# Optimization experiments

Hardware: AMD Instinct MI355X
Metric: run time of the kernel (lower is better)

## Reference

```python
import jax, jax.numpy as jnp
import numpy as np

B, C, H, W = 16, 192, 48, 48
EPS = 1e-5  # torch LayerNorm default


def setup_inputs() -> dict:
    key = jax.random.key(0)
    ks = jax.random.split(key, 5)
    dim = C
    x = jax.random.normal(ks[0], (B, C, H, W), dtype=jnp.float32)
    ln_w = jnp.ones((dim,), dtype=jnp.float32)
    ln_b = jnp.zeros((dim,), dtype=jnp.float32)
    s = 1.0 / np.sqrt(dim)
    Wq = jax.random.uniform(ks[1], (dim, dim), jnp.float32, -s, s)
    Wk = jax.random.uniform(ks[2], (dim, dim), jnp.float32, -s, s)
    Wv = jax.random.uniform(ks[3], (dim, dim), jnp.float32, -s, s)
    w1 = jnp.ones((1,), dtype=jnp.float32)
    w2 = jnp.ones((1,), dtype=jnp.float32)
    return {"x": x, "ln_w": ln_w, "ln_b": ln_b, "Wq": Wq, "Wk": Wk, "Wv": Wv, "w1": w1, "w2": w2}


def reference(x, ln_w, ln_b, Wq, Wk, Wv, w1, w2):
    b, c, h, w = x.shape
    # [B, C, H, W] -> [B, N, C]
    xf = x.reshape(b, c, h * w).transpose(0, 2, 1)
    # LayerNorm over channel dim
    mu = jnp.mean(xf, axis=-1, keepdims=True)
    var = jnp.mean(jnp.square(xf - mu), axis=-1, keepdims=True)
    xn = (xf - mu) * jax.lax.rsqrt(var + EPS) * ln_w + ln_b
    # torch Linear: y = x @ W^T
    Q = jnp.einsum('bnc,dc->bnd', xn, Wq)
    K = jnp.einsum('bnc,dc->bnd', xn, Wk)
    V = jnp.einsum('bnc,dc->bnd', xn, Wv)
    S = jnp.einsum('bnd,bmd->bnm', Q, K)  # [B, N, N]
    attn1 = jax.nn.softmax(S, axis=-1)
    attn2 = jnp.square(jax.nn.relu(S))
    # learned blend weights (softmax over two scalars)
    e1, e2 = jnp.exp(w1), jnp.exp(w2)
    denom = e1 + e2
    attn = (e1 / denom) * attn1 + (e2 / denom) * attn2
    out = jnp.einsum('bnm,bmd->bnd', attn, V)  # [B, N, C]
    out = out.transpose(0, 2, 1).reshape(b, c, h, w)
    return out + x
```

## Files before the change

### kernel.cpp

```cpp
#include <hip/hip_runtime.h>

#define NN 2304
#define CC 192
#define NBATCH 16

typedef unsigned short u16;
typedef __bf16 bf16x8 __attribute__((ext_vector_type(8)));
typedef float f32x4 __attribute__((ext_vector_type(4)));
typedef float f32x16 __attribute__((ext_vector_type(16)));

__device__ __forceinline__ u16 bf16bits(float f) {
  union { float f; unsigned u; } v;
  v.f = f;
  unsigned r = v.u + 0x7FFFu + ((v.u >> 16) & 1u);
  return (u16)(r >> 16);
}

__device__ __forceinline__ uint32_t cvtpk(float lo, float hi) {
  uint32_t d;
  asm("v_cvt_pk_bf16_f32 %0, %1, %2" : "=v"(d) : "v"(lo), "v"(hi));
  return d;
}

__device__ __forceinline__ int swzK(int row, int col) {
  int ch = col >> 3;
  int phys = (ch & ~7) | ((ch ^ row) & 7);
  return row * 192 + (phys << 3) + (col & 7);
}
__device__ __forceinline__ int swz64(int row, int col) {
  int ch = (col >> 3) ^ row;
  return (row << 6) | ((ch & 7) << 3) | (col & 7);
}

__device__ __forceinline__ void gll16(const u16* g, u16* l) {
  __builtin_amdgcn_global_load_lds(
      (const __attribute__((address_space(1))) u16*)g,
      (__attribute__((address_space(3))) u16*)l, 16, 0, 0);
}

__global__ __launch_bounds__(256) void ln_kernel(
    const float* __restrict__ x, const float* __restrict__ lnw,
    const float* __restrict__ lnb, u16* __restrict__ xn) {
  __shared__ float xt[192 * 65];
  __shared__ float psum[4][64], psq[4][64];
  __shared__ float mu_s[64], rs_s[64];
  __shared__ float lw_s[192], lb_s[192];
  int t = threadIdx.x;
  int b = blockIdx.y, n0 = blockIdx.x * 64;
  const float* xb = x + (size_t)b * CC * NN;
  if (t < 192) { lw_s[t] = lnw[t]; lb_s[t] = lnb[t]; }
#pragma unroll
  for (int i = 0; i < 48; ++i) {
    int idx = i * 256 + t;
    int c = idx >> 6, n = idx & 63;
    xt[c * 65 + n] = xb[(size_t)c * NN + n0 + n];
  }
  __syncthreads();
  {
    int n = t & 63, part = t >> 6;
    float s = 0.f, s2 = 0.f;
#pragma unroll
    for (int c = part * 48; c < part * 48 + 48; ++c) {
      float v = xt[c * 65 + n];
      s += v; s2 += v * v;
    }
    psum[part][n] = s; psq[part][n] = s2;
  }
  __syncthreads();
  if (t < 64) {
    float s = psum[0][t] + psum[1][t] + psum[2][t] + psum[3][t];
    float s2 = psq[0][t] + psq[1][t] + psq[2][t] + psq[3][t];
    float mu = s * (1.0f / 192.0f);
    float var = s2 * (1.0f / 192.0f) - mu * mu;
    mu_s[t] = mu;
    rs_s[t] = rsqrtf(var + 1e-5f);
  }
  __syncthreads();
#pragma unroll
  for (int i = 0; i < 12; ++i) {
    int u = i * 256 + t;
    int n = u / 48, cq = (u % 48) * 4;
    float mu = mu_s[n], rs = rs_s[n];
    float v0 = (xt[(cq + 0) * 65 + n] - mu) * rs * lw_s[cq + 0] + lb_s[cq + 0];
    float v1 = (xt[(cq + 1) * 65 + n] - mu) * rs * lw_s[cq + 1] + lb_s[cq + 1];
    float v2 = (xt[(cq + 2) * 65 + n] - mu) * rs * lw_s[cq + 2] + lb_s[cq + 2];
    float v3 = (xt[(cq + 3) * 65 + n] - mu) * rs * lw_s[cq + 3] + lb_s[cq + 3];
    uint2 o;
    o.x = cvtpk(v0, v1);
    o.y = cvtpk(v2, v3);
    *(uint2*)&xn[((size_t)(b * NN + n0 + n)) * CC + cq] = o;
  }
}

__global__ __launch_bounds__(256) void wconv_kernel(
    const float* __restrict__ Wq, const float* __restrict__ Wk,
    const float* __restrict__ Wv, u16* __restrict__ wbf) {
  int z = blockIdx.y;
  const float* W = (z == 0) ? Wq : (z == 1 ? Wk : Wv);
  u16* o = wbf + (size_t)z * 36864;
  int idx = (blockIdx.x * 256 + (int)threadIdx.x) * 8;
  float4 f0 = *(const float4*)&W[idx];
  float4 f1 = *(const float4*)&W[idx + 4];
  uint4 v;
  v.x = cvtpk(f0.x, f0.y);
  v.y = cvtpk(f0.z, f0.w);
  v.z = cvtpk(f1.x, f1.y);
  v.w = cvtpk(f1.z, f1.w);
  *(uint4*)&o[idx] = v;
}

__global__ __launch_bounds__(256, 3) void qkv_gemm(
    const u16* __restrict__ xn, const u16* __restrict__ wbf,
    u16* __restrict__ qb, u16* __restrict__ kb, u16* __restrict__ vtb) {
  __shared__ u16 xs[12288];
  __shared__ u16 wsm[12288];
  int t = threadIdx.x, w = t >> 6, lane = t & 63, l15 = lane & 15, qd = lane >> 4;
  int m0 = blockIdx.x * 64, n0 = blockIdx.y * 64;

#pragma unroll
  for (int i = 0; i < 6; ++i) {
    int cid = i * 4 + w, sc = cid * 64 + lane;
    int row = sc / 24, pc = sc % 24;
    int gc = (pc & ~7) | ((pc ^ row) & 7);
    gll16(xn + (size_t)(m0 + row) * 192 + gc * 8, xs + cid * 512);
  }
#pragma unroll
  for (int i = 0; i < 6; ++i) {
    int cid = i * 4 + w, sc = cid * 64 + lane;
    int row = sc / 24, pc = sc % 24;
    int gc = (pc & ~7) | ((pc ^ row) & 7);
    gll16(wbf + (size_t)(n0 + row) * 192 + gc * 8, wsm + cid * 512);
  }

  bf16x8 a[6];
  const f32x4 fz = {0.f, 0.f, 0.f, 0.f};
  for (int z = 0; z < 3; ++z) {
    asm volatile("s_waitcnt vmcnt(0) lgkmcnt(0)\ns_barrier" ::: "memory");
    if (z == 0) {
#pragma unroll
      for (int kk = 0; kk < 6; ++kk)
        a[kk] = *(const bf16x8*)&xs[swzK(w * 16 + l15, kk * 32 + qd * 8)];
    }
    f32x4 acc[4];
#pragma unroll
    for (int ct = 0; ct < 4; ++ct) {
      acc[ct] = fz;
#pragma unroll
      for (int kk = 0; kk < 6; ++kk) {
        bf16x8 bfr = *(const bf16x8*)&wsm[swzK(ct * 16 + l15, kk * 32 + qd * 8)];
        acc[ct] = __builtin_amdgcn_mfma_f32_16x16x32_bf16(a[kk], bfr, acc[ct], 0, 0, 0);
      }
    }
    asm volatile("s_waitcnt lgkmcnt(0)\ns_barrier" ::: "memory");
    if (z < 2) {
#pragma unroll
      for (int i = 0; i < 6; ++i) {
        int cid = i * 4 + w, sc = cid * 64 + lane;
        int row = sc / 24, pc = sc % 24;
        int gc = (pc & ~7) | ((pc ^ row) & 7);
        gll16(wbf + (size_t)(z + 1) * 36864 + (size_t)(n0 + row) * 192 + gc * 8,
              wsm + cid * 512);
      }
      u16* outp = (z == 0) ? qb : kb;
#pragma unroll
      for (int ct = 0; ct < 4; ++ct)
#pragma unroll
        for (int r = 0; r < 4; ++r) {
          int m = m0 + w * 16 + qd * 4 + r;
          outp[(size_t)m * 192 + n0 + ct * 16 + l15] = bf16bits(acc[ct][r]);
        }
    } else {
#pragma unroll
      for (int ct = 0; ct < 4; ++ct)
#pragma unroll
        for (int r = 0; r < 4; ++r)
          xs[swz64(ct * 16 + l15, w * 16 + qd * 4 + r)] = bf16bits(acc[ct][r]);
      __syncthreads();
      int bb = blockIdx.x / 36, nb = (blockIdx.x % 36) * 64;
#pragma unroll
      for (int i = 0; i < 16; ++i) {
        int idx = i * 256 + t;
        int d = idx >> 6, nn = idx & 63;
        vtb[(size_t)bb * 192 * NN + (size_t)(n0 + d) * NN + nb + nn] = xs[swz64(d, nn)];
      }
    }
  }
}

__global__ __launch_bounds__(256, 2) void attn_fused(
    const u16* __restrict__ qb, const u16* __restrict__ kb,
    const u16* __restrict__ vtb, const float* __restrict__ w1p,
    const float* __restrict__ w2p, const float* __restrict__ x,
    float* __restrict__ out) {
  __shared__ u16 sm[32768];
  float* olds = (float*)sm;
  float* lred = (float*)(sm + 24576);

  int t = threadIdx.x, w = t >> 6, lane = t & 63;
  int l31 = lane & 31, hi = lane >> 5;
  int qh = w >> 1, ch = w & 1;
  int bid = blockIdx.x;
  int xcd = bid & 7, j = bid >> 3;
  int b = xcd * 2 + (j >= 36 ? 1 : 0);
  int qt = (j >= 36) ? j - 36 : j;

  const u16* Kg = kb + (size_t)b * NN * CC;
  const u16* Vg = vtb + (size_t)b * CC * NN;
  const u16* Qr = qb + ((size_t)b * NN + qt * 64 + qh * 32 + l31) * CC + hi * 8;
  bf16x8 qf[12];
#pragma unroll
  for (int ks = 0; ks < 12; ++ks) qf[ks] = *(const bf16x8*)(Qr + ks * 16);

  float e1 = __expf(w1p[0]), e2 = __expf(w2p[0]);
  float den = e1 + e2;
  float c1f = e1 / den, c2f = e2 / den;

  u16* pexSW = sm + 24576 + (qh * 2 + ch) * 1024 + lane * 8;
  const u16* pexSR = sm + 24576 + (qh * 2 + (1 - ch)) * 1024 + lane * 8;
  u16* pexRW = sm + 28672 + (qh * 2 + ch) * 1024 + lane * 8;
  const u16* pexRR = sm + 28672 + (qh * 2 + (1 - ch)) * 1024 + lane * 8;

  f32x16 z16;
#pragma unroll
  for (int i = 0; i < 16; ++i) z16[i] = 0.f;
  f32x16 os[3], orl[3];
#pragma unroll
  for (int i = 0; i < 3; ++i) { os[i] = z16; orl[i] = z16; }
  float lsum = 0.f;

#define STAGE_K(KT)                                                        \
  {                                                                        \
    _Pragma("unroll") for (int i = 0; i < 6; ++i) {                        \
      int cid = i * 4 + w, sc = cid * 64 + lane;                           \
      int row = sc / 24, pc = sc % 24;                                     \
      int gc = (pc & ~7) | ((pc ^ row) & 7);                               \
      gll16(Kg + ((size_t)(KT) * 64 + row) * CC + gc * 8, sm + cid * 512); \
    }                                                                      \
  }
#define STAGE_V(KT)                                                        \
  {                                                                        \
    _Pragma("unroll") for (int i = 0; i < 6; ++i) {                        \
      int cid = i * 4 + w, sc = cid * 64 + lane;                           \
      int d = sc >> 3, pc = sc & 7, gc = (pc ^ d) & 7;                     \
      gll16(Vg + (size_t)d * NN + (KT) * 64 + gc * 8,                      \
            sm + 12288 + cid * 512);                                       \
    }                                                                      \
  }

  alignas(16) uint32_t pS0[4], pS1[4], pR0[4], pR1[4];
#define S_BLEND()                                                           \
  {                                                                         \
    f32x16 sA0 = z16, sA1 = z16;                                            \
    __builtin_amdgcn_s_setprio(1);                                          \
    _Pragma("unroll") for (int ks = 0; ks < 6; ++ks) {                      \
      bf16x8 k0 =                                                           \
          *(const bf16x8*)&sm[swzK(ch * 32 + l31, (2 * ks) * 16 + hi * 8)]; \
      bf16x8 k1 =                                                           \
          *(const bf16x8*)&sm[swzK(ch * 32 + l31, (2 * ks + 1) * 16 + hi * 8)]; \
      sA0 = __builtin_amdgcn_mfma_f32_32x32x16_bf16(k0, qf[2 * ks], sA0, 0, 0, 0); \
      sA1 = __builtin_amdgcn_mfma_f32_32x32x16_bf16(k1, qf[2 * ks + 1], sA1, 0, 0, 0); \
    }                                                                       \
    __builtin_amdgcn_s_setprio(0);                                          \
    uint32_t WS[8], WR[8];                                                  \
    _Pragma("unroll") for (int g = 0; g < 4; ++g) {                         \
      float sv0 = sA0[4 * g + 0] + sA1[4 * g + 0];                          \
      float sv1 = sA0[4 * g + 1] + sA1[4 * g + 1];                          \
      float sv2 = sA0[4 * g + 2] + sA1[4 * g + 2];                          \
      float sv3 = sA0[4 * g + 3] + sA1[4 * g + 3];                          \
      float e0 = __expf(fminf(sv0, 60.f));                                  \
      float e1v = __expf(fminf(sv1, 60.f));                                 \
      float e2v = __expf(fminf(sv2, 60.f));                                 \
      float e3 = __expf(fminf(sv3, 60.f));                                  \
      float r0 = fmaxf(sv0, 0.f), r1 = fmaxf(sv1, 0.f);                     \
      float r2 = fmaxf(sv2, 0.f), r3 = fmaxf(sv3, 0.f);                     \
      lsum += (e0 + e1v) + (e2v + e3);                                      \
      WS[2 * g] = cvtpk(e0, e1v);                                           \
      WS[2 * g + 1] = cvtpk(e2v, e3);                                       \
      WR[2 * g] = cvtpk(r0 * r0, r1 * r1);                                  \
      WR[2 * g + 1] = cvtpk(r2 * r2, r3 * r3);                              \
    }                                                                       \
    uint32_t XS[8], XR[8];                                                  \
    _Pragma("unroll") for (int jj = 0; jj < 8; ++jj) {                      \
      XS[jj] = __shfl_xor(WS[jj], 32);                                      \
      XR[jj] = __shfl_xor(WR[jj], 32);                                      \
    }                                                                       \
    pS0[0] = hi ? XS[2] : WS[0]; pS0[1] = hi ? XS[3] : WS[1];               \
    pS0[2] = hi ? WS[2] : XS[0]; pS0[3] = hi ? WS[3] : XS[1];               \
    pS1[0] = hi ? XS[6] : WS[4]; pS1[1] = hi ? XS[7] : WS[5];               \
    pS1[2] = hi ? WS[6] : XS[4]; pS1[3] = hi ? WS[7] : XS[5];               \
    pR0[0] = hi ? XR[2] : WR[0]; pR0[1] = hi ? XR[3] : WR[1];               \
    pR0[2] = hi ? WR[2] : XR[0]; pR0[3] = hi ? WR[3] : XR[1];               \
    pR1[0] = hi ? XR[6] : WR[4]; pR1[1] = hi ? XR[7] : WR[5];               \
    pR1[2] = hi ? WR[6] : XR[4]; pR1[3] = hi ? WR[7] : XR[5];               \
    *(uint4*)pexSW = *(uint4*)pS0;                                          \
    *(uint4*)(pexSW + 512) = *(uint4*)pS1;                                  \
    *(uint4*)pexRW = *(uint4*)pR0;                                          \
    *(uint4*)(pexRW + 512) = *(uint4*)pR1;                                  \
  }

  STAGE_K(0);
  STAGE_V(0);
  asm volatile("s_waitcnt vmcnt(6)\ns_barrier" ::: "memory");
  S_BLEND();
  asm volatile("s_waitcnt lgkmcnt(0)\ns_barrier" ::: "memory");
  STAGE_K(1);

  for (int kt = 0; kt < 36; ++kt) {
    if (kt == 35)
      asm volatile("s_waitcnt vmcnt(0) lgkmcnt(0)\ns_barrier" ::: "memory");
    else
      asm volatile("s_waitcnt vmcnt(6) lgkmcnt(0)\ns_barrier" ::: "memory");

    const u16* vl = sm + 12288;
    uint4 sS0 = *(const uint4*)pexSR;
    uint4 sS1 = *(const uint4*)(pexSR + 512);
    uint4 sR0 = *(const uint4*)pexRR;
    uint4 sR1 = *(const uint4*)(pexRR + 512);
    __builtin_amdgcn_s_setprio(1);
#pragma unroll
    for (int dt = 0; dt < 3; ++dt) {
      int d = ch * 96 + dt * 32 + l31;
      bf16x8 vo0 = *(const bf16x8*)&vl[swz64(d, (ch * 2 + 0) * 16 + hi * 8)];
      bf16x8 vo1 = *(const bf16x8*)&vl[swz64(d, (ch * 2 + 1) * 16 + hi * 8)];
      bf16x8 vs0 = *(const bf16x8*)&vl[swz64(d, ((1 - ch) * 2 + 0) * 16 + hi * 8)];
      bf16x8 vs1 = *(const bf16x8*)&vl[swz64(d, ((1 - ch) * 2 + 1) * 16 + hi * 8)];
      os[dt] = __builtin_amdgcn_mfma_f32_32x32x16_bf16(
          *(const bf16x8*)pS0, vo0, os[dt], 0, 0, 0);
      orl[dt] = __builtin_amdgcn_mfma_f32_32x32x16_bf16(
          *(const bf16x8*)pR0, vo0, orl[dt], 0, 0, 0);
      os[dt] = __builtin_amdgcn_mfma_f32_32x32x16_bf16(
          *(const bf16x8*)pS1, vo1, os[dt], 0, 0, 0);
      orl[dt] = __builtin_amdgcn_mfma_f32_32x32x16_bf16(
          *(const bf16x8*)pR1, vo1, orl[dt], 0, 0, 0);
      os[dt] = __builtin_amdgcn_mfma_f32_32x32x16_bf16(
          *(const bf16x8*)&sS0, vs0, os[dt], 0, 0, 0);
      orl[dt] = __builtin_amdgcn_mfma_f32_32x32x16_bf16(
          *(const bf16x8*)&sR0, vs0, orl[dt], 0, 0, 0);
      os[dt] = __builtin_amdgcn_mfma_f32_32x32x16_bf16(
          *(const bf16x8*)&sS1, vs1, os[dt], 0, 0, 0);
      orl[dt] = __builtin_amdgcn_mfma_f32_32x32x16_bf16(
          *(const bf16x8*)&sR1, vs1, orl[dt], 0, 0, 0);
    }
    __builtin_amdgcn_s_setprio(0);

    if (kt < 35) {
      asm volatile("s_waitcnt vmcnt(0) lgkmcnt(0)\ns_barrier" ::: "memory");
      STAGE_V(kt + 1);
      S_BLEND();
      asm volatile("s_waitcnt lgkmcnt(0)\ns_barrier" ::: "memory");
      if (kt + 2 < 36) STAGE_K(kt + 2);
    }
  }

  lsum += __shfl_xor(lsum, 32);
  __syncthreads();
  if (lane < 32) lred[(qh * 2 + ch) * 32 + l31] = lsum;
  __syncthreads();
  float linv[16];
#pragma unroll
  for (int r = 0; r < 16; ++r) {
    int m = (r & 3) + 8 * (r >> 2) + 4 * hi;
    float ltot = lred[(qh * 2 + 0) * 32 + m] + lred[(qh * 2 + 1) * 32 + m];
    linv[r] = c1f / ltot;
  }
  __syncthreads();
#pragma unroll
  for (int dt = 0; dt < 3; ++dt) {
    int d = ch * 96 + dt * 32 + l31;
#pragma unroll
    for (int r = 0; r < 16; ++r) {
      int m = (r & 3) + 8 * (r >> 2) + 4 * hi;
      int q = qh * 32 + m;
      olds[d * 64 + ((q & ~31) | ((q ^ d) & 31))] =
          os[dt][r] * linv[r] + c2f * orl[dt][r];
    }
  }
  __syncthreads();
  const float* xb = x + (size_t)b * CC * NN + qt * 64;
  float* ob = out + (size_t)b * CC * NN + qt * 64;
#pragma unroll
  for (int i = 0; i < 48; ++i) {
    int idx = i * 256 + t;
    int c = idx >> 6, nn = idx & 63;
    float v = olds[c * 64 + ((nn & ~31) | ((nn ^ c) & 31))];
    ob[(size_t)c * NN + nn] = v + xb[(size_t)c * NN + nn];
  }
#undef STAGE_K
#undef STAGE_V
#undef S_BLEND
}

extern "C" void kernel_launch(void* const* d_in, const int* in_sizes, int n_in,
                              void* d_out, int out_size, void* d_ws, size_t ws_size,
                              hipStream_t stream) {
  (void)in_sizes; (void)n_in; (void)out_size; (void)ws_size;
  const float* x   = (const float*)d_in[0];
  const float* lnw = (const float*)d_in[1];
  const float* lnb = (const float*)d_in[2];
  const float* Wq  = (const float*)d_in[3];
  const float* Wk  = (const float*)d_in[4];
  const float* Wv  = (const float*)d_in[5];
  const float* w1  = (const float*)d_in[6];
  const float* w2  = (const float*)d_in[7];
  float* out = (float*)d_out;

  u16* xn = (u16*)d_ws;
  size_t per = (size_t)NBATCH * NN * CC;
  u16* qb  = xn + per;
  u16* kb  = qb + per;
  u16* vtb = kb + per;
  u16* wbf = vtb + per;

  ln_kernel<<<dim3(36, 16), 256, 0, stream>>>(x, lnw, lnb, xn);
  wconv_kernel<<<dim3(18, 3), 256, 0, stream>>>(Wq, Wk, Wv, wbf);
  qkv_gemm<<<dim3(576, 3), 256, 0, stream>>>(xn, wbf, qb, kb, vtb);
  attn_fused<<<dim3(576), 256, 0, stream>>>(qb, kb, vtb, w1, w2, x, out);
}
```

Measured before the change: 285.9 us.

## Make attention kernel persistent with per-XCD atomic tile scheduler

The attention kernel now launches 512 persistent blocks instead of 576 one-shot blocks. Each block repeatedly claims a query tile from a per-XCD atomic counter, which keeps each XCD's work within its two batches for L2 locality. The intent is to remove the tail effect where 576 blocks do not divide evenly over 256 CUs × 2 blocks, and to balance load dynamically. It adds a memset, atomic traffic and an extra barrier per tile, and it needs workspace space for the counters.

```diff
diff --git a/kernel.cpp b/kernel.cpp
--- a/kernel.cpp
+++ b/kernel.cpp
@@ -191,25 +191,16 @@
     const u16* __restrict__ qb, const u16* __restrict__ kb,
     const u16* __restrict__ vtb, const float* __restrict__ w1p,
     const float* __restrict__ w2p, const float* __restrict__ x,
-    float* __restrict__ out) {
+    float* __restrict__ out, unsigned* __restrict__ cnt) {
   __shared__ u16 sm[32768];
+  __shared__ int tile_s;
   float* olds = (float*)sm;
   float* lred = (float*)(sm + 24576);
 
   int t = threadIdx.x, w = t >> 6, lane = t & 63;
   int l31 = lane & 31, hi = lane >> 5;
   int qh = w >> 1, ch = w & 1;
-  int bid = blockIdx.x;
-  int xcd = bid & 7, j = bid >> 3;
-  int b = xcd * 2 + (j >= 36 ? 1 : 0);
-  int qt = (j >= 36) ? j - 36 : j;
-
-  const u16* Kg = kb + (size_t)b * NN * CC;
-  const u16* Vg = vtb + (size_t)b * CC * NN;
-  const u16* Qr = qb + ((size_t)b * NN + qt * 64 + qh * 32 + l31) * CC + hi * 8;
-  bf16x8 qf[12];
-#pragma unroll
-  for (int ks = 0; ks < 12; ++ks) qf[ks] = *(const bf16x8*)(Qr + ks * 16);
+  int g = blockIdx.x & 7;
 
   float e1 = __expf(w1p[0]), e2 = __expf(w2p[0]);
   float den = e1 + e2;
@@ -223,10 +214,6 @@
   f32x16 z16;
 #pragma unroll
   for (int i = 0; i < 16; ++i) z16[i] = 0.f;
-  f32x16 os[3], orl[3];
-#pragma unroll
-  for (int i = 0; i < 3; ++i) { os[i] = z16; orl[i] = z16; }
-  float lsum = 0.f;
 
 #define STAGE_K(KT)                                                        \
   {                                                                        \
@@ -247,7 +234,6 @@
     }                                                                      \
   }
 
-  alignas(16) uint32_t pS0[4], pS1[4], pR0[4], pR1[4];
 #define S_BLEND()                                                           \
   {                                                                         \
     f32x16 sA0 = z16, sA1 = z16;                                            \
@@ -262,11 +248,11 @@
     }                                                                       \
     __builtin_amdgcn_s_setprio(0);                                          \
     uint32_t WS[8], WR[8];                                                  \
-    _Pragma("unroll") for (int g = 0; g < 4; ++g) {                         \
-      float sv0 = sA0[4 * g + 0] + sA1[4 * g + 0];                          \
-      float sv1 = sA0[4 * g + 1] + sA1[4 * g + 1];                          \
-      float sv2 = sA0[4 * g + 2] + sA1[4 * g + 2];                          \
-      float sv3 = sA0[4 * g + 3] + sA1[4 * g + 3];                          \
+    _Pragma("unroll") for (int gg = 0; gg < 4; ++gg) {                      \
+      float sv0 = sA0[4 * gg + 0] + sA1[4 * gg + 0];                        \
+      float sv1 = sA0[4 * gg + 1] + sA1[4 * gg + 1];                        \
+      float sv2 = sA0[4 * gg + 2] + sA1[4 * gg + 2];                        \
+      float sv3 = sA0[4 * gg + 3] + sA1[4 * gg + 3];                        \
       float e0 = __expf(fminf(sv0, 60.f));                                  \
       float e1v = __expf(fminf(sv1, 60.f));                                 \
       float e2v = __expf(fminf(sv2, 60.f));                                 \
@@ -274,10 +260,10 @@
       float r0 = fmaxf(sv0, 0.f), r1 = fmaxf(sv1, 0.f);                     \
       float r2 = fmaxf(sv2, 0.f), r3 = fmaxf(sv3, 0.f);                     \
       lsum += (e0 + e1v) + (e2v + e3);                                      \
-      WS[2 * g] = cvtpk(e0, e1v);                                           \
-      WS[2 * g + 1] = cvtpk(e2v, e3);                                       \
-      WR[2 * g] = cvtpk(r0 * r0, r1 * r1);                                  \
-      WR[2 * g + 1] = cvtpk(r2 * r2, r3 * r3);                              \
+      WS[2 * gg] = cvtpk(e0, e1v);                                          \
+      WS[2 * gg + 1] = cvtpk(e2v, e3);                                      \
+      WR[2 * gg] = cvtpk(r0 * r0, r1 * r1);                                 \
+      WR[2 * gg + 1] = cvtpk(r2 * r2, r3 * r3);                             \
     }                                                                       \
     uint32_t XS[8], XR[8];                                                  \
     _Pragma("unroll") for (int jj = 0; jj < 8; ++jj) {                      \
@@ -298,92 +284,114 @@
     *(uint4*)(pexRW + 512) = *(uint4*)pR1;                                  \
   }
 
-  STAGE_K(0);
-  STAGE_V(0);
-  asm volatile("s_waitcnt vmcnt(6)\ns_barrier" ::: "memory");
-  S_BLEND();
-  asm volatile("s_waitcnt lgkmcnt(0)\ns_barrier" ::: "memory");
-  STAGE_K(1);
-
-  for (int kt = 0; kt < 36; ++kt) {
-    if (kt == 35)
-      asm volatile("s_waitcnt vmcnt(0) lgkmcnt(0)\ns_barrier" ::: "memory");
-    else
-      asm volatile("s_waitcnt vmcnt(6) lgkmcnt(0)\ns_barrier" ::: "memory");
-
-    const u16* vl = sm + 12288;
-    uint4 sS0 = *(const uint4*)pexSR;
-    uint4 sS1 = *(const uint4*)(pexSR + 512);
-    uint4 sR0 = *(const uint4*)pexRR;
-    uint4 sR1 = *(const uint4*)(pexRR + 512);
-    __builtin_amdgcn_s_setprio(1);
+  for (;;) {
+    if (t == 0) tile_s = (int)atomicAdd(&cnt[g], 1u);
+    __syncthreads();
+    int tl = tile_s;
+    if (tl >= 72) break;
+    int b = g * 2 + (tl >= 36 ? 1 : 0);
+    int qt = (tl >= 36) ? tl - 36 : tl;
+
+    const u16* Kg = kb + (size_t)b * NN * CC;
+    const u16* Vg = vtb + (size_t)b * CC * NN;
+    const u16* Qr = qb + ((size_t)b * NN + qt * 64 + qh * 32 + l31) * CC + hi * 8;
+    bf16x8 qf[12];
+#pragma unroll
+    for (int ks = 0; ks < 12; ++ks) qf[ks] = *(const bf16x8*)(Qr + ks * 16);
+
+    f32x16 os[3], orl[3];
+#pragma unroll
+    for (int i = 0; i < 3; ++i) { os[i] = z16; orl[i] = z16; }
+    float lsum = 0.f;
+    alignas(16) uint32_t pS0[4], pS1[4], pR0[4], pR1[4];
+
+    STAGE_K(0);
+    STAGE_V(0);
+    asm volatile("s_waitcnt vmcnt(6)\ns_barrier" ::: "memory");
+    S_BLEND();
+    asm volatile("s_waitcnt lgkmcnt(0)\ns_barrier" ::: "memory");
+    STAGE_K(1);
+
+    for (int kt = 0; kt < 36; ++kt) {
+      if (kt == 35)
+        asm volatile("s_waitcnt vmcnt(0) lgkmcnt(0)\ns_barrier" ::: "memory");
+      else
+        asm volatile("s_waitcnt vmcnt(6) lgkmcnt(0)\ns_barrier" ::: "memory");
+
+      const u16* vl = sm + 12288;
+      uint4 sS0 = *(const uint4*)pexSR;
+      uint4 sS1 = *(const uint4*)(pexSR + 512);
+      uint4 sR0 = *(const uint4*)pexRR;
+      uint4 sR1 = *(const uint4*)(pexRR + 512);
+      __builtin_amdgcn_s_setprio(1);
+#pragma unroll
+      for (int dt = 0; dt < 3; ++dt) {
+        int d = ch * 96 + dt * 32 + l31;
+        bf16x8 vo0 = *(const bf16x8*)&vl[swz64(d, (ch * 2 + 0) * 16 + hi * 8)];
+        bf16x8 vo1 = *(const bf16x8*)&vl[swz64(d, (ch * 2 + 1) * 16 + hi * 8)];
+        bf16x8 vs0 = *(const bf16x8*)&vl[swz64(d, ((1 - ch) * 2 + 0) * 16 + hi * 8)];
+        bf16x8 vs1 = *(const bf16x8*)&vl[swz64(d, ((1 - ch) * 2 + 1) * 16 + hi * 8)];
+        os[dt] = __builtin_amdgcn_mfma_f32_32x32x16_bf16(
+            *(const bf16x8*)pS0, vo0, os[dt], 0, 0, 0);
+        orl[dt] = __builtin_amdgcn_mfma_f32_32x32x16_bf16(
+            *(const bf16x8*)pR0, vo0, orl[dt], 0, 0, 0);
+        os[dt] = __builtin_amdgcn_mfma_f32_32x32x16_bf16(
+            *(const bf16x8*)pS1, vo1, os[dt], 0, 0, 0);
+        orl[dt] = __builtin_amdgcn_mfma_f32_32x32x16_bf16(
+            *(const bf16x8*)pR1, vo1, orl[dt], 0, 0, 0);
+        os[dt] = __builtin_amdgcn_mfma_f32_32x32x16_bf16(
+            *(const bf16x8*)&sS0, vs0, os[dt], 0, 0, 0);
+        orl[dt] = __builtin_amdgcn_mfma_f32_32x32x16_bf16(
+            *(const bf16x8*)&sR0, vs0, orl[dt], 0, 0, 0);
+        os[dt] = __builtin_amdgcn_mfma_f32_32x32x16_bf16(
+            *(const bf16x8*)&sS1, vs1, os[dt], 0, 0, 0);
+        orl[dt] = __builtin_amdgcn_mfma_f32_32x32x16_bf16(
+            *(const bf16x8*)&sR1, vs1, orl[dt], 0, 0, 0);
+      }
+      __builtin_amdgcn_s_setprio(0);
+
+      if (kt < 35) {
+        asm volatile("s_waitcnt vmcnt(0) lgkmcnt(0)\ns_barrier" ::: "memory");
+        STAGE_V(kt + 1);
+        S_BLEND();
+        asm volatile("s_waitcnt lgkmcnt(0)\ns_barrier" ::: "memory");
+        if (kt + 2 < 36) STAGE_K(kt + 2);
+      }
+    }
+
+    lsum += __shfl_xor(lsum, 32);
+    __syncthreads();
+    if (lane < 32) lred[(qh * 2 + ch) * 32 + l31] = lsum;
+    __syncthreads();
+    float linv[16];
+#pragma unroll
+    for (int r = 0; r < 16; ++r) {
+      int m = (r & 3) + 8 * (r >> 2) + 4 * hi;
+      float ltot = lred[(qh * 2 + 0) * 32 + m] + lred[(qh * 2 + 1) * 32 + m];
+      linv[r] = c1f / ltot;
+    }
+    __syncthreads();
 #pragma unroll
     for (int dt = 0; dt < 3; ++dt) {
       int d = ch * 96 + dt * 32 + l31;
-      bf16x8 vo0 = *(const bf16x8*)&vl[swz64(d, (ch * 2 + 0) * 16 + hi * 8)];
-      bf16x8 vo1 = *(const bf16x8*)&vl[swz64(d, (ch * 2 + 1) * 16 + hi * 8)];
-      bf16x8 vs0 = *(const bf16x8*)&vl[swz64(d, ((1 - ch) * 2 + 0) * 16 + hi * 8)];
-      bf16x8 vs1 = *(const bf16x8*)&vl[swz64(d, ((1 - ch) * 2 + 1) * 16 + hi * 8)];
-      os[dt] = __builtin_amdgcn_mfma_f32_32x32x16_bf16(
-          *(const bf16x8*)pS0, vo0, os[dt], 0, 0, 0);
-      orl[dt] = __builtin_amdgcn_mfma_f32_32x32x16_bf16(
-          *(const bf16x8*)pR0, vo0, orl[dt], 0, 0, 0);
-      os[dt] = __builtin_amdgcn_mfma_f32_32x32x16_bf16(
-          *(const bf16x8*)pS1, vo1, os[dt], 0, 0, 0);
-      orl[dt] = __builtin_amdgcn_mfma_f32_32x32x16_bf16(
-          *(const bf16x8*)pR1, vo1, orl[dt], 0, 0, 0);
-      os[dt] = __builtin_amdgcn_mfma_f32_32x32x16_bf16(
-          *(const bf16x8*)&sS0, vs0, os[dt], 0, 0, 0);
-      orl[dt] = __builtin_amdgcn_mfma_f32_32x32x16_bf16(
-          *(const bf16x8*)&sR0, vs0, orl[dt], 0, 0, 0);
-      os[dt] = __builtin_amdgcn_mfma_f32_32x32x16_bf16(
-          *(const bf16x8*)&sS1, vs1, os[dt], 0, 0, 0);
-      orl[dt] = __builtin_amdgcn_mfma_f32_32x32x16_bf16(
-          *(const bf16x8*)&sR1, vs1, orl[dt], 0, 0, 0);
-    }
-    __builtin_amdgcn_s_setprio(0);
-
-    if (kt < 35) {
-      asm volatile("s_waitcnt vmcnt(0) lgkmcnt(0)\ns_barrier" ::: "memory");
-      STAGE_V(kt + 1);
-      S_BLEND();
-      asm volatile("s_waitcnt lgkmcnt(0)\ns_barrier" ::: "memory");
-      if (kt + 2 < 36) STAGE_K(kt + 2);
-    }
-  }
-
-  lsum += __shfl_xor(lsum, 32);
-  __syncthreads();
-  if (lane < 32) lred[(qh * 2 + ch) * 32 + l31] = lsum;
-  __syncthreads();
-  float linv[16];
-#pragma unroll
-  for (int r = 0; r < 16; ++r) {
-    int m = (r & 3) + 8 * (r >> 2) + 4 * hi;
-    float ltot = lred[(qh * 2 + 0) * 32 + m] + lred[(qh * 2 + 1) * 32 + m];
-    linv[r] = c1f / ltot;
-  }
-  __syncthreads();
-#pragma unroll
-  for (int dt = 0; dt < 3; ++dt) {
-    int d = ch * 96 + dt * 32 + l31;
-#pragma unroll
-    for (int r = 0; r < 16; ++r) {
-      int m = (r & 3) + 8 * (r >> 2) + 4 * hi;
-      int q = qh * 32 + m;
-      olds[d * 64 + ((q & ~31) | ((q ^ d) & 31))] =
-          os[dt][r] * linv[r] + c2f * orl[dt][r];
-    }
-  }
-  __syncthreads();
-  const float* xb = x + (size_t)b * CC * NN + qt * 64;
-  float* ob = out + (size_t)b * CC * NN + qt * 64;
-#pragma unroll
-  for (int i = 0; i < 48; ++i) {
-    int idx = i * 256 + t;
-    int c = idx >> 6, nn = idx & 63;
-    float v = olds[c * 64 + ((nn & ~31) | ((nn ^ c) & 31))];
-    ob[(size_t)c * NN + nn] = v + xb[(size_t)c * NN + nn];
+#pragma unroll
+      for (int r = 0; r < 16; ++r) {
+        int m = (r & 3) + 8 * (r >> 2) + 4 * hi;
+        int q = qh * 32 + m;
+        olds[d * 64 + ((q & ~31) | ((q ^ d) & 31))] =
+            os[dt][r] * linv[r] + c2f * orl[dt][r];
+      }
+    }
+    __syncthreads();
+    const float* xb = x + (size_t)b * CC * NN + qt * 64;
+    float* ob = out + (size_t)b * CC * NN + qt * 64;
+#pragma unroll
+    for (int i = 0; i < 48; ++i) {
+      int idx = i * 256 + t;
+      int c = idx >> 6, nn = idx & 63;
+      float v = olds[c * 64 + ((nn & ~31) | ((nn ^ c) & 31))];
+      ob[(size_t)c * NN + nn] = v + xb[(size_t)c * NN + nn];
+    }
   }
 #undef STAGE_K
 #undef STAGE_V
@@ -410,9 +418,11 @@
   u16* kb  = qb + per;
   u16* vtb = kb + per;
   u16* wbf = vtb + per;
+  unsigned* cnt = (unsigned*)(wbf + 3 * 36864);
 
   ln_kernel<<<dim3(36, 16), 256, 0, stream>>>(x, lnw, lnb, xn);
   wconv_kernel<<<dim3(18, 3), 256, 0, stream>>>(Wq, Wk, Wv, wbf);
   qkv_gemm<<<dim3(576, 3), 256, 0, stream>>>(xn, wbf, qb, kb, vtb);
-  attn_fused<<<dim3(576), 256, 0, stream>>>(qb, kb, vtb, w1, w2, x, out);
-}
+  hipMemsetAsync(cnt, 0, 8 * sizeof(unsigned), stream);
+  attn_fused<<<dim3(512), 256, 0, stream>>>(qb, kb, vtb, w1, w2, x, out, cnt);
+}
```

After: 403.3 us. 1.41x slower.
